# Optimization experiments

Hardware: AMD Instinct MI355X
Metric: run time of the kernel (lower is better)

## Reference

```python
import jax, jax.numpy as jnp
import numpy as np

N_NODES = 100000
N_EDGES = 600000
D_IN = 128
D_OUT = 128


def setup_inputs() -> dict:
    key = jax.random.key(0)
    k1, k2, k3 = jax.random.split(key, 3)
    x = jax.random.normal(k1, (N_NODES, D_IN), dtype=jnp.float32)
    edge_index = jax.random.randint(k2, (2, N_EDGES), 0, N_NODES, dtype=jnp.int32)
    W = jax.random.normal(k3, (D_OUT, D_IN), dtype=jnp.float32) * 0.02
    b = jnp.zeros((D_OUT,), dtype=jnp.float32)
    return {"x": x, "edge_index": edge_index, "W": W, "b": b}


def reference(x, edge_index, W, b):
    # x: [N, D], edge_index: [2, E]
    n = x.shape[0]
    src = edge_index[0]
    dst = edge_index[1]
    # gather + elementwise abs diff: [E, D]
    msg = jnp.abs(x[src] - x[dst])
    # scatter-mean with out=x.clone(): sum includes the initial x values,
    # count is the number of scattered edges per node. Self-loops add a zero
    # message and +1 to the count, so counts = out_degree + 1 >= 1.
    sums = x + jax.ops.segment_sum(msg, src, num_segments=n)
    counts = jax.ops.segment_sum(jnp.ones_like(src, dtype=x.dtype), src, num_segments=n) + 1.0
    out = sums / counts[:, None]
    # Linear
    return out @ W.T + b
```

## Files before the change

kernel.cpp:

```cpp
#include <hip/hip_runtime.h>

#define D 128
#define CHB 8
#define CHSZ 256
#define TILE 2048
#define CAPCH 1856
#define SCAN_N 512
#define CAPQ 960
#define MAXDEG 32

typedef __attribute__((ext_vector_type(8))) short bf16x8;
typedef __attribute__((ext_vector_type(4))) short bf16x4;
typedef __attribute__((ext_vector_type(4))) unsigned short u16x4;
typedef __attribute__((ext_vector_type(4))) float f32x4;

__device__ inline short f2bf(float f) {
    unsigned u = __float_as_uint(f);
    unsigned r = (u + 0x7fff + ((u >> 16) & 1)) >> 16;
    return (short)r;
}
__device__ inline bf16x8 pack8(float4 a, float4 b) {
    bf16x8 r;
    r[0] = f2bf(a.x); r[1] = f2bf(a.y); r[2] = f2bf(a.z); r[3] = f2bf(a.w);
    r[4] = f2bf(b.x); r[5] = f2bf(b.y); r[6] = f2bf(b.z); r[7] = f2bf(b.w);
    return r;
}
__device__ inline float bf2f(unsigned short h) {
    return __uint_as_float(((unsigned)h) << 16);
}

__global__ __launch_bounds__(256) void zero_ints(int* __restrict__ g, int n) {
    int i = blockIdx.x * 256 + threadIdx.x;
    if (i < n) g[i] = 0;
}

__global__ __launch_bounds__(256) void prep3(const float* __restrict__ x,
                                             unsigned short* __restrict__ xh,
                                             const int* __restrict__ ei,
                                             int* __restrict__ gcur,
                                             int2* __restrict__ part,
                                             const float* __restrict__ Wg,
                                             bf16x8* __restrict__ Wpk,
                                             int N, int E, int NT, int NCH) {
    __shared__ int hist[SCAN_N];
    __shared__ int pref[SCAN_N];
    __shared__ int gbase[SCAN_N];
    __shared__ int2 sedge[TILE];
    int t = threadIdx.x;
    if ((int)blockIdx.x < NT) {
        int e0 = blockIdx.x * TILE;
        int cntT = E - e0; if (cntT > TILE) cntT = TILE;
        for (int i = t; i < SCAN_N; i += 256) hist[i] = 0;
        __syncthreads();

        int src[8], dst[8], rk[8];
        int base8 = e0 + t * 8;
        if (base8 + 8 <= E) {
            int4 s0 = *(const int4*)(ei + base8);
            int4 s1 = *(const int4*)(ei + base8 + 4);
            int4 d0 = *(const int4*)(ei + E + base8);
            int4 d1 = *(const int4*)(ei + E + base8 + 4);
            src[0]=s0.x; src[1]=s0.y; src[2]=s0.z; src[3]=s0.w;
            src[4]=s1.x; src[5]=s1.y; src[6]=s1.z; src[7]=s1.w;
            dst[0]=d0.x; dst[1]=d0.y; dst[2]=d0.z; dst[3]=d0.w;
            dst[4]=d1.x; dst[5]=d1.y; dst[6]=d1.z; dst[7]=d1.w;
        } else {
#pragma unroll
            for (int k = 0; k < 8; ++k) {
                int g = base8 + k;
                src[k] = (g < E) ? ei[g] : 0;
                dst[k] = (g < E) ? ei[E + g] : 0;
            }
        }
#pragma unroll
        for (int k = 0; k < 8; ++k) {
            rk[k] = (t * 8 + k < cntT) ? atomicAdd(&hist[src[k] >> CHB], 1) : -1;
        }
        __syncthreads();
        if (t == 0) {
            int acc = 0;
            for (int i = 0; i < SCAN_N; ++i) { pref[i] = acc; acc += hist[i]; }
        }
        __syncthreads();
        for (int c = t; c < NCH; c += 256)
            gbase[c] = hist[c] ? atomicAdd(&gcur[c], hist[c]) : 0;
#pragma unroll
        for (int k = 0; k < 8; ++k)
            if (rk[k] >= 0)
                sedge[pref[src[k] >> CHB] + rk[k]] = make_int2(src[k], dst[k]);
        __syncthreads();
        for (int i = t; i < cntT; i += 256) {
            int2 e = sedge[i];
            int c = e.x >> CHB;
            int slot = gbase[c] + (i - pref[c]);
            if (slot < CAPCH) part[(size_t)c * CAPCH + slot] = e;
        }
    } else if ((int)blockIdx.x == NT) {
        for (int i = t; i < 2048; i += 256) {
            int f = i >> 6, l = i & 63;
            int n16 = f >> 2, kk = f & 3;
            int c = n16 * 16 + (l & 15);
            int k0 = kk * 32 + (l >> 4) * 8;
            float4 p0 = *(const float4*)(Wg + c * D + k0);
            float4 p1 = *(const float4*)(Wg + c * D + k0 + 4);
            Wpk[i] = pack8(p0, p1);
        }
    } else {
        long idx = (long)(blockIdx.x - NT - 1) * 256 + t;
        long total = (long)N * D / 8;
        if (idx < total) {
            const float4* xp = (const float4*)x;
            float4 p0 = xp[idx * 2];
            float4 p1 = xp[idx * 2 + 1];
            ((bf16x8*)xh)[idx] = pack8(p0, p1);
        }
    }
}

__global__ __launch_bounds__(256) void aggcsr(const unsigned short* __restrict__ xh,
                                              const int* __restrict__ gcur,
                                              const int2* __restrict__ part,
                                              unsigned short* __restrict__ yh,
                                              int N) {
    __shared__ int nh[64];
    __shared__ int off[65];
    __shared__ int adj[CAPQ];
    int t = threadIdx.x;
    int ch = blockIdx.x >> 2;
    int sub = blockIdx.x & 3;
    int nbase = (ch << CHB) + sub * 64;
    int cnt = gcur[ch]; if (cnt > CAPCH) cnt = CAPCH;
    if (t < 64) nh[t] = 0;
    __syncthreads();

    int2 e2[8]; int rk2[8];
#pragma unroll
    for (int ii = 0; ii < 8; ++ii) {
        int i = ii * 256 + t;
        rk2[ii] = -1;
        if (i < cnt) {
            int2 e = part[(size_t)ch * CAPCH + i];
            int rl = e.x & (CHSZ - 1);
            if ((rl >> 6) == sub) {
                e2[ii] = e;
                rk2[ii] = atomicAdd(&nh[rl & 63], 1);
            }
        }
    }
    __syncthreads();
    if (t == 0) {
        int acc = 0;
        for (int i = 0; i < 64; ++i) { off[i] = acc; acc += nh[i]; }
        off[64] = acc;
    }
    __syncthreads();
#pragma unroll
    for (int ii = 0; ii < 8; ++ii)
        if (rk2[ii] >= 0) {
            int idx = off[e2[ii].x & 63] + rk2[ii];
            if (idx < CAPQ) adj[idx] = e2[ii].y;
        }
    __syncthreads();

    int team = t >> 5, lane = t & 31;
    for (int rl = team; rl < 64; rl += 8) {
        int r = nbase + rl;
        if (r >= N) continue;
        int deg = nh[rl];
        int ab = off[rl];
        int dg = deg;
        if (ab + dg > CAPQ) dg = CAPQ - ab;
        if (dg < 0) dg = 0;
        u16x4 ah = *(const u16x4*)(xh + (size_t)r * D + lane * 4);
        float4 a;
        a.x = bf2f(ah[0]); a.y = bf2f(ah[1]); a.z = bf2f(ah[2]); a.w = bf2f(ah[3]);
        float4 a0 = a;
        float4 a1 = {0, 0, 0, 0}, a2 = {0, 0, 0, 0}, a3 = {0, 0, 0, 0};
        for (int f = 0; f < dg; f += 4) {
            int d0 = adj[ab + f];
            int d1 = (f + 1 < dg) ? adj[ab + f + 1] : r;
            int d2 = (f + 2 < dg) ? adj[ab + f + 2] : r;
            int d3 = (f + 3 < dg) ? adj[ab + f + 3] : r;
            u16x4 v0 = *(const u16x4*)(xh + (size_t)d0 * D + lane * 4);
            u16x4 v1 = *(const u16x4*)(xh + (size_t)d1 * D + lane * 4);
            u16x4 v2 = *(const u16x4*)(xh + (size_t)d2 * D + lane * 4);
            u16x4 v3 = *(const u16x4*)(xh + (size_t)d3 * D + lane * 4);
            a0.x += fabsf(a.x - bf2f(v0[0])); a0.y += fabsf(a.y - bf2f(v0[1]));
            a0.z += fabsf(a.z - bf2f(v0[2])); a0.w += fabsf(a.w - bf2f(v0[3]));
            a1.x += fabsf(a.x - bf2f(v1[0])); a1.y += fabsf(a.y - bf2f(v1[1]));
            a1.z += fabsf(a.z - bf2f(v1[2])); a1.w += fabsf(a.w - bf2f(v1[3]));
            a2.x += fabsf(a.x - bf2f(v2[0])); a2.y += fabsf(a.y - bf2f(v2[1]));
            a2.z += fabsf(a.z - bf2f(v2[2])); a2.w += fabsf(a.w - bf2f(v2[3]));
            a3.x += fabsf(a.x - bf2f(v3[0])); a3.y += fabsf(a.y - bf2f(v3[1]));
            a3.z += fabsf(a.z - bf2f(v3[2])); a3.w += fabsf(a.w - bf2f(v3[3]));
        }
        float s = 1.0f / (float)(deg + 1);
        bf16x4 p;
        p[0] = f2bf(((a0.x + a1.x) + (a2.x + a3.x)) * s);
        p[1] = f2bf(((a0.y + a1.y) + (a2.y + a3.y)) * s);
        p[2] = f2bf(((a0.z + a1.z) + (a2.z + a3.z)) * s);
        p[3] = f2bf(((a0.w + a1.w) + (a2.w + a3.w)) * s);
        *(bf16x4*)(yh + (size_t)r * D + lane * 4) = p;
    }
}

__global__ __launch_bounds__(256) void mfma_v2(const unsigned short* __restrict__ yh,
                                               const bf16x8* __restrict__ Wpk,
                                               const float* __restrict__ bvec,
                                               float* __restrict__ out, int N, int RB) {
    int cg = blockIdx.x / RB;
    int rg = blockIdx.x % RB;
    int w = threadIdx.x >> 6;
    int l = threadIdx.x & 63;
    int rw = w >> 1, cw = w & 1;
    int l15 = l & 15, lk8 = (l >> 4) * 8;
    int rowbase = rg * 64 + rw * 32;
    int col16 = cg * 2 + cw;
    int c = col16 * 16 + l15;

    bf16x8 Af[2][4];
#pragma unroll
    for (int m = 0; m < 2; ++m) {
        int r = rowbase + m * 16 + l15;
        int rc = r < N ? r : N - 1;
#pragma unroll
        for (int kk = 0; kk < 4; ++kk)
            Af[m][kk] = *(const bf16x8*)(yh + (size_t)rc * D + kk * 32 + lk8);
    }

    f32x4 acc0 = {}, acc1 = {};
#pragma unroll
    for (int kk = 0; kk < 4; ++kk) {
        bf16x8 Bf = Wpk[(col16 * 4 + kk) * 64 + l];
        acc0 = __builtin_amdgcn_mfma_f32_16x16x32_bf16(Af[0][kk], Bf, acc0, 0, 0, 0);
        acc1 = __builtin_amdgcn_mfma_f32_16x16x32_bf16(Af[1][kk], Bf, acc1, 0, 0, 0);
    }

    float bias = bvec[c];
#pragma unroll
    for (int m = 0; m < 2; ++m) {
        f32x4 acc = m ? acc1 : acc0;
        int r0 = rowbase + m * 16 + (l >> 4) * 4;
#pragma unroll
        for (int j = 0; j < 4; ++j) {
            int r = r0 + j;
            if (r < N) out[(size_t)r * D + c] = acc[j] + bias;
        }
    }
}

__global__ __launch_bounds__(256) void bucket_fb(const int* __restrict__ ei,
                                                 int* __restrict__ cnt,
                                                 int* __restrict__ bucket, int E) {
    int e = blockIdx.x * 256 + threadIdx.x;
    if (e >= E) return;
    int src = ei[e];
    int dst = ei[E + e];
    int pos = atomicAdd(&cnt[src], 1);
    if (pos < MAXDEG) bucket[src * MAXDEG + pos] = dst;
}

__global__ __launch_bounds__(256) void agg_f32(const float* __restrict__ x,
                                               const int* __restrict__ cnt,
                                               const int* __restrict__ bucket,
                                               float* __restrict__ y, int N) {
    int t = blockIdx.x * 256 + threadIdx.x;
    int team = t >> 5;
    int lane = t & 31;
    if (team >= N) return;
    int r = team;
    int deg = cnt[r];
    float4 a = ((const float4*)(x + (size_t)r * D))[lane];
    int m = deg < MAXDEG ? deg : MAXDEG;
    const int* bk = bucket + (size_t)r * MAXDEG;
    float4 a0 = a, a1 = {0,0,0,0}, a2 = {0,0,0,0}, a3 = {0,0,0,0};
    for (int j = 0; j < m; j += 4) {
        int4 d4 = *(const int4*)(bk + j);
        int d0 = d4.x;
        int d1 = (j + 1 < m) ? d4.y : r;
        int d2 = (j + 2 < m) ? d4.z : r;
        int d3 = (j + 3 < m) ? d4.w : r;
        float4 v0 = ((const float4*)(x + (size_t)d0 * D))[lane];
        float4 v1 = ((const float4*)(x + (size_t)d1 * D))[lane];
        float4 v2 = ((const float4*)(x + (size_t)d2 * D))[lane];
        float4 v3 = ((const float4*)(x + (size_t)d3 * D))[lane];
        a0.x += fabsf(a.x - v0.x); a0.y += fabsf(a.y - v0.y);
        a0.z += fabsf(a.z - v0.z); a0.w += fabsf(a.w - v0.w);
        a1.x += fabsf(a.x - v1.x); a1.y += fabsf(a.y - v1.y);
        a1.z += fabsf(a.z - v1.z); a1.w += fabsf(a.w - v1.w);
        a2.x += fabsf(a.x - v2.x); a2.y += fabsf(a.y - v2.y);
        a2.z += fabsf(a.z - v2.z); a2.w += fabsf(a.w - v2.w);
        a3.x += fabsf(a.x - v3.x); a3.y += fabsf(a.y - v3.y);
        a3.z += fabsf(a.z - v3.z); a3.w += fabsf(a.w - v3.w);
    }
    float s = 1.0f / (float)(deg + 1);
    float4 o;
    o.x = ((a0.x + a1.x) + (a2.x + a3.x)) * s;
    o.y = ((a0.y + a1.y) + (a2.y + a3.y)) * s;
    o.z = ((a0.z + a1.z) + (a2.z + a3.z)) * s;
    o.w = ((a0.w + a1.w) + (a2.w + a3.w)) * s;
    ((float4*)(y + (size_t)r * D))[lane] = o;
}

__global__ __launch_bounds__(256) void mfma_f32(const float* y,
                                                const float* __restrict__ W,
                                                const float* __restrict__ b,
                                                float* out, int N) {
    int w = threadIdx.x >> 6;
    int l = threadIdx.x & 63;
    int rw = w >> 1;
    int cw = w & 1;
    int l15 = l & 15;
    int lk8 = (l >> 4) * 8;
    bf16x8 Bf[4][4];
    float bias[4];
#pragma unroll
    for (int n = 0; n < 4; ++n) {
        int c = cw * 64 + n * 16 + l15;
        const float* wr = W + c * D;
        bias[n] = b[c];
#pragma unroll
        for (int kk = 0; kk < 4; ++kk) {
            float4 p0 = *(const float4*)(wr + kk * 32 + lk8);
            float4 p1 = *(const float4*)(wr + kk * 32 + lk8 + 4);
            Bf[n][kk] = pack8(p0, p1);
        }
    }
    int rowbase = blockIdx.x * 64 + rw * 32;
    bf16x8 Af[2][4];
#pragma unroll
    for (int m = 0; m < 2; ++m) {
        int r = rowbase + m * 16 + l15;
        int rc = r < N ? r : N - 1;
        const float* yr = y + (size_t)rc * D;
#pragma unroll
        for (int kk = 0; kk < 4; ++kk) {
            float4 p0 = *(const float4*)(yr + kk * 32 + lk8);
            float4 p1 = *(const float4*)(yr + kk * 32 + lk8 + 4);
            Af[m][kk] = pack8(p0, p1);
        }
    }
    f32x4 acc[2][4] = {};
#pragma unroll
    for (int m = 0; m < 2; ++m)
#pragma unroll
        for (int n = 0; n < 4; ++n)
#pragma unroll
            for (int kk = 0; kk < 4; ++kk)
                acc[m][n] = __builtin_amdgcn_mfma_f32_16x16x32_bf16(
                    Af[m][kk], Bf[n][kk], acc[m][n], 0, 0, 0);
#pragma unroll
    for (int m = 0; m < 2; ++m) {
        int r0 = rowbase + m * 16 + (l >> 4) * 4;
#pragma unroll
        for (int n = 0; n < 4; ++n) {
            int c = cw * 64 + n * 16 + l15;
#pragma unroll
            for (int j = 0; j < 4; ++j) {
                int r = r0 + j;
                if (r < N) out[(size_t)r * D + c] = acc[m][n][j] + bias[n];
            }
        }
    }
}

extern "C" void kernel_launch(void* const* d_in, const int* in_sizes, int n_in,
                              void* d_out, int out_size, void* d_ws, size_t ws_size,
                              hipStream_t stream) {
    const float* x  = (const float*)d_in[0];
    const int*   ei = (const int*)d_in[1];
    const float* W  = (const float*)d_in[2];
    const float* b  = (const float*)d_in[3];
    float* out = (float*)d_out;

    int N = in_sizes[0] / D;
    int E = in_sizes[1] / 2;

    int NCH = (N + CHSZ - 1) >> CHB;
    int NT  = (E + TILE - 1) / TILE;
    int RB  = (N + 63) / 64;

    char* ws = (char*)d_ws;
    unsigned short* yh = (unsigned short*)ws;
    int2* part = (int2*)(ws + (size_t)N * D * 2);
    int* gcur = (int*)(part + (size_t)NCH * CAPCH);
    size_t wpo = (((size_t)((char*)(gcur + NCH) - ws)) + 255) & ~(size_t)255;
    bf16x8* Wpk = (bf16x8*)(ws + wpo);
    size_t need = wpo + 32768;

    bool ok = (ws_size >= need) && (NCH <= SCAN_N) &&
              ((size_t)out_size * 4 >= (size_t)N * D * 2);

    if (ok) {
        unsigned short* xh = (unsigned short*)d_out;

        zero_ints<<<(NCH + 255) / 256, 256, 0, stream>>>(gcur, NCH);
        long conv_threads = (long)N * D / 8;
        int cblocks = (int)((conv_threads + 255) / 256);
        prep3<<<NT + 1 + cblocks, 256, 0, stream>>>(x, xh, ei, gcur, part, W, Wpk,
                                                    N, E, NT, NCH);
        aggcsr<<<NCH * 4, 256, 0, stream>>>(xh, gcur, part, yh, N);
        mfma_v2<<<RB * 4, 256, 0, stream>>>(yh, Wpk, b, out, N, RB);
    } else {
        int* cnt    = (int*)d_ws;
        int* bucket = cnt + N;
        int teams_per_block = 256 / 32;
        int ablocks = (N + teams_per_block - 1) / teams_per_block;
        zero_ints<<<(N + 255) / 256, 256, 0, stream>>>(cnt, N);
        bucket_fb<<<(E + 255) / 256, 256, 0, stream>>>(ei, cnt, bucket, E);
        agg_f32<<<ablocks, 256, 0, stream>>>(x, cnt, bucket, out, N);
        mfma_f32<<<(N + 63) / 64, 256, 0, stream>>>(out, W, b, out, N);
    }
}
```

Baseline: 96.55 us.

## Fuse aggregation and MFMA linear layer via LDS tile, drop yh round trip

Merges the aggregation kernel and the bf16 MFMA matmul into one kernel. Each block writes its 64 aggregated rows into a padded LDS tile and multiplies them by the packed W in place, so the bf16 intermediate no longer goes to global memory and one launch is removed. The bf16 copy of x now lives in workspace instead of the output buffer. In exchange each wave computes 4 column tiles, which raises register use, and the 17KB LDS tile may reduce occupancy of the gather-bound phase.

```diff
diff --git a/kernel.cpp b/kernel.cpp
--- a/kernel.cpp
+++ b/kernel.cpp
@@ -7,6 +7,7 @@
 #define CAPCH 1856
 #define SCAN_N 512
 #define CAPQ 960
+#define PADW 136
 #define MAXDEG 32
 
 typedef __attribute__((ext_vector_type(8))) short bf16x8;
@@ -117,14 +118,16 @@
     }
 }
 
-__global__ __launch_bounds__(256) void aggcsr(const unsigned short* __restrict__ xh,
-                                              const int* __restrict__ gcur,
-                                              const int2* __restrict__ part,
-                                              unsigned short* __restrict__ yh,
-                                              int N) {
+__global__ __launch_bounds__(256) void aggmm(const unsigned short* __restrict__ xh,
+                                             const int* __restrict__ gcur,
+                                             const int2* __restrict__ part,
+                                             const bf16x8* __restrict__ Wpk,
+                                             const float* __restrict__ bvec,
+                                             float* __restrict__ out, int N) {
     __shared__ int nh[64];
     __shared__ int off[65];
     __shared__ int adj[CAPQ];
+    __shared__ __align__(16) short tile[64 * PADW];
     int t = threadIdx.x;
     int ch = blockIdx.x >> 2;
     int sub = blockIdx.x & 3;
@@ -165,7 +168,8 @@
     int team = t >> 5, lane = t & 31;
     for (int rl = team; rl < 64; rl += 8) {
         int r = nbase + rl;
-        if (r >= N) continue;
+        bf16x4* lp = (bf16x4*)&tile[rl * PADW + lane * 4];
+        if (r >= N) { bf16x4 z = {0, 0, 0, 0}; *lp = z; continue; }
         int deg = nh[rl];
         int ab = off[rl];
         int dg = deg;
@@ -200,51 +204,49 @@
         p[1] = f2bf(((a0.y + a1.y) + (a2.y + a3.y)) * s);
         p[2] = f2bf(((a0.z + a1.z) + (a2.z + a3.z)) * s);
         p[3] = f2bf(((a0.w + a1.w) + (a2.w + a3.w)) * s);
-        *(bf16x4*)(yh + (size_t)r * D + lane * 4) = p;
-    }
-}
-
-__global__ __launch_bounds__(256) void mfma_v2(const unsigned short* __restrict__ yh,
-                                               const bf16x8* __restrict__ Wpk,
-                                               const float* __restrict__ bvec,
-                                               float* __restrict__ out, int N, int RB) {
-    int cg = blockIdx.x / RB;
-    int rg = blockIdx.x % RB;
-    int w = threadIdx.x >> 6;
-    int l = threadIdx.x & 63;
+        *lp = p;
+    }
+
+    __syncthreads();
+
+    int w = t >> 6;
+    int l = t & 63;
     int rw = w >> 1, cw = w & 1;
     int l15 = l & 15, lk8 = (l >> 4) * 8;
-    int rowbase = rg * 64 + rw * 32;
-    int col16 = cg * 2 + cw;
-    int c = col16 * 16 + l15;
 
     bf16x8 Af[2][4];
 #pragma unroll
     for (int m = 0; m < 2; ++m) {
-        int r = rowbase + m * 16 + l15;
-        int rc = r < N ? r : N - 1;
+        int row = rw * 32 + m * 16 + l15;
 #pragma unroll
         for (int kk = 0; kk < 4; ++kk)
-            Af[m][kk] = *(const bf16x8*)(yh + (size_t)rc * D + kk * 32 + lk8);
-    }
-
-    f32x4 acc0 = {}, acc1 = {};
-#pragma unroll
-    for (int kk = 0; kk < 4; ++kk) {
-        bf16x8 Bf = Wpk[(col16 * 4 + kk) * 64 + l];
-        acc0 = __builtin_amdgcn_mfma_f32_16x16x32_bf16(Af[0][kk], Bf, acc0, 0, 0, 0);
-        acc1 = __builtin_amdgcn_mfma_f32_16x16x32_bf16(Af[1][kk], Bf, acc1, 0, 0, 0);
-    }
-
-    float bias = bvec[c];
+            Af[m][kk] = *(const bf16x8*)&tile[row * PADW + kk * 32 + lk8];
+    }
+
+    f32x4 acc[2][4] = {};
+#pragma unroll
+    for (int n = 0; n < 4; ++n) {
+        int col16 = cw * 4 + n;
+#pragma unroll
+        for (int kk = 0; kk < 4; ++kk) {
+            bf16x8 Bf = Wpk[(col16 * 4 + kk) * 64 + l];
+            acc[0][n] = __builtin_amdgcn_mfma_f32_16x16x32_bf16(Af[0][kk], Bf, acc[0][n], 0, 0, 0);
+            acc[1][n] = __builtin_amdgcn_mfma_f32_16x16x32_bf16(Af[1][kk], Bf, acc[1][n], 0, 0, 0);
+        }
+    }
+
 #pragma unroll
     for (int m = 0; m < 2; ++m) {
-        f32x4 acc = m ? acc1 : acc0;
-        int r0 = rowbase + m * 16 + (l >> 4) * 4;
-#pragma unroll
-        for (int j = 0; j < 4; ++j) {
-            int r = r0 + j;
-            if (r < N) out[(size_t)r * D + c] = acc[j] + bias;
+        int r0 = nbase + rw * 32 + m * 16 + (l >> 4) * 4;
+#pragma unroll
+        for (int n = 0; n < 4; ++n) {
+            int c = cw * 64 + n * 16 + l15;
+            float bias = bvec[c];
+#pragma unroll
+            for (int j = 0; j < 4; ++j) {
+                int r = r0 + j;
+                if (r < N) out[(size_t)r * D + c] = acc[m][n][j] + bias;
+            }
         }
     }
 }
@@ -378,29 +380,24 @@
 
     int NCH = (N + CHSZ - 1) >> CHB;
     int NT  = (E + TILE - 1) / TILE;
-    int RB  = (N + 63) / 64;
 
     char* ws = (char*)d_ws;
-    unsigned short* yh = (unsigned short*)ws;
+    unsigned short* xh = (unsigned short*)ws;
     int2* part = (int2*)(ws + (size_t)N * D * 2);
     int* gcur = (int*)(part + (size_t)NCH * CAPCH);
     size_t wpo = (((size_t)((char*)(gcur + NCH) - ws)) + 255) & ~(size_t)255;
     bf16x8* Wpk = (bf16x8*)(ws + wpo);
     size_t need = wpo + 32768;
 
-    bool ok = (ws_size >= need) && (NCH <= SCAN_N) &&
-              ((size_t)out_size * 4 >= (size_t)N * D * 2);
+    bool ok = (ws_size >= need) && (NCH <= SCAN_N);
 
     if (ok) {
-        unsigned short* xh = (unsigned short*)d_out;
-
         zero_ints<<<(NCH + 255) / 256, 256, 0, stream>>>(gcur, NCH);
         long conv_threads = (long)N * D / 8;
         int cblocks = (int)((conv_threads + 255) / 256);
         prep3<<<NT + 1 + cblocks, 256, 0, stream>>>(x, xh, ei, gcur, part, W, Wpk,
                                                     N, E, NT, NCH);
-        aggcsr<<<NCH * 4, 256, 0, stream>>>(xh, gcur, part, yh, N);
-        mfma_v2<<<RB * 4, 256, 0, stream>>>(yh, Wpk, b, out, N, RB);
+        aggmm<<<NCH * 4, 256, 0, stream>>>(xh, gcur, part, Wpk, b, out, N);
     } else {
         int* cnt    = (int*)d_ws;
         int* bucket = cnt + N;
```

Result: faster. 82.82 us (-14.2%).
